# Kernel tuning notes

Hardware: AMD Instinct MI355X
Metric: run time of the kernel (lower is better)

The kernel has to match this reference:

```python
import jax, jax.numpy as jnp
import numpy as np

N = 50000      # nodes
E = 800000     # edges (avg degree 16)
D_IN, D_H, D_OUT = 128, 128, 64
EPS = 1e-5


def setup_inputs() -> dict:
    key = jax.random.key(0)
    ks = jax.random.split(key, 6)
    feat = jax.random.normal(ks[0], (N, D_IN), dtype=jnp.float32)
    # Consistent CSR adjacency: sorted destination rows -> nodePointer via searchsorted
    rows = np.sort(np.asarray(jax.random.randint(ks[1], (E,), 0, N, dtype=jnp.int32)))
    edge_rows = jnp.asarray(rows, dtype=jnp.int32)              # [E] destination node per edge
    nodePointer = jnp.asarray(np.searchsorted(rows, np.arange(N + 1)), dtype=jnp.int32)  # [N+1]
    edgeList = jax.random.randint(ks[2], (E,), 0, N, dtype=jnp.int32)  # [E] source (column) indices
    def glorot(k, i, o):
        return jax.random.normal(k, (i, o), dtype=jnp.float32) * (1.0 / np.sqrt(i)).astype(np.float32)
    W0 = glorot(ks[3], D_IN, D_H)
    W1 = glorot(ks[4], D_H, D_H)
    W2 = glorot(ks[5], D_H, D_OUT)
    return {"feat": feat, "W0": W0, "W1": W1, "W2": W2,
            "nodePointer": nodePointer, "edgeList": edgeList, "edge_rows": edge_rows}


def _layer_norm(x):
    # Fresh nn.LayerNorm each forward in the original => weight=1, bias=0
    mu = jnp.mean(x, axis=-1, keepdims=True)
    var = jnp.mean(jnp.square(x - mu), axis=-1, keepdims=True)
    return (x - mu) * jax.lax.rsqrt(var + EPS)


def reference(feat, W0, W1, W2, nodePointer, edgeList, edge_rows):
    h = feat
    Ws = [W0, W1, W2]
    n_layers = len(Ws)
    for l, W in enumerate(Ws):
        xw = h @ W                      # [N, d_out] dense GEMM
        msg = xw[edgeList]              # [E, d_out] gather source-node features
        h = jax.ops.segment_sum(msg, edge_rows, num_segments=N)  # SpMM: A @ (h W)
        h = _layer_norm(h)
        if l != n_layers - 1:
            h = jax.nn.relu(h)
    return h
```

## Files before the change

### kernel.cpp

```cpp
#include <hip/hip_runtime.h>
#include <cstddef>


typedef __attribute__((ext_vector_type(8))) short bf16x8;
typedef __attribute__((ext_vector_type(4))) float floatx4;
typedef __attribute__((ext_vector_type(4))) unsigned int uintx4;
typedef __attribute__((ext_vector_type(2))) unsigned int uintx2;

static __device__ __forceinline__ unsigned int f2bf(float f) {
    union { float f; unsigned int u; } v; v.f = f;
    unsigned int u = v.u;
    u += 0x7fffu + ((u >> 16) & 1u);
    return u >> 16;
}
static __device__ __forceinline__ float bf_lo(unsigned int p) {
    union { unsigned int u; float f; } v; v.u = p << 16; return v.f;
}
static __device__ __forceinline__ float bf_hi(unsigned int p) {
    union { unsigned int u; float f; } v; v.u = p & 0xffff0000u; return v.f;
}
static __device__ __forceinline__ void acc8(float* a, uintx4 v) {
    a[0] += bf_lo(v.x); a[1] += bf_hi(v.x);
    a[2] += bf_lo(v.y); a[3] += bf_hi(v.y);
    a[4] += bf_lo(v.z); a[5] += bf_hi(v.z);
    a[6] += bf_lo(v.w); a[7] += bf_hi(v.w);
}
static __device__ __forceinline__ void acc4(float* a, uintx2 v) {
    a[0] += bf_lo(v.x); a[1] += bf_hi(v.x);
    a[2] += bf_lo(v.y); a[3] += bf_hi(v.y);
}

__global__ __launch_bounds__(256) void cvt_w(const float* __restrict__ W0,
                                             const float* __restrict__ W1,
                                             const float* __restrict__ W2,
                                             unsigned int* __restrict__ WtF) {
    const int m = blockIdx.x >> 4;
    const int slice = blockIdx.x & 15;
    const float* W = (m == 0) ? W0 : (m == 1) ? W1 : W2;
    const int ncols = (m == 2) ? 64 : 128;
    unsigned int* dst = WtF + m * 128 * 64;
    const int total = ncols * 64;
    for (int idx = slice * 256 + threadIdx.x; idx < total; idx += 16 * 256) {
        const int j    = idx & 3;
        const int lane = (idx >> 2) & 63;
        const int s    = (idx >> 8) & 3;
        const int t    = idx >> 10;
        const int mcol = lane & 15;
        const int quad = lane >> 4;
        const int n = t * 16 + mcol;
        const int k = s * 32 + quad * 8 + 2 * j;
        unsigned int lo = f2bf(W[(size_t)k * ncols + n]);
        unsigned int hi = f2bf(W[(size_t)(k + 1) * ncols + n]);
        dst[idx] = (hi << 16) | lo;
    }
}

template <int NCOLS, bool A_FP32>
__global__ __launch_bounds__(64) void gemm_mfma(const void* __restrict__ Av,
                                                const unsigned int* __restrict__ Wt,
                                                unsigned int* __restrict__ C,
                                                int M) {
    const int lane = threadIdx.x;
    const int row0 = blockIdx.x * 16;
    const int quad = lane >> 4;
    const int mcol = lane & 15;

    constexpr int NT = NCOLS / 16;
    floatx4 acc[NT];
    #pragma unroll
    for (int t = 0; t < NT; ++t) acc[t] = (floatx4){0.f, 0.f, 0.f, 0.f};

    int aidx = row0 + mcol; if (aidx >= M) aidx = M - 1;
    const float*        arowF = (const float*)Av + (size_t)aidx * 128 + quad * 8;
    const unsigned int* afrag = (const unsigned int*)Av + (size_t)blockIdx.x * 1024 + lane * 4;
    const unsigned int* bbase = Wt + lane * 4;

    #pragma unroll
    for (int s = 0; s < 4; ++s) {
        bf16x8 a;
        if constexpr (A_FP32) {
            float4 fa = *(const float4*)(arowF + s * 32);
            float4 fb = *(const float4*)(arowF + s * 32 + 4);
            uintx4 ap;
            ap.x = (f2bf(fa.y) << 16) | f2bf(fa.x);
            ap.y = (f2bf(fa.w) << 16) | f2bf(fa.z);
            ap.z = (f2bf(fb.y) << 16) | f2bf(fb.x);
            ap.w = (f2bf(fb.w) << 16) | f2bf(fb.z);
            a = __builtin_bit_cast(bf16x8, ap);
        } else {
            uintx4 ap = *(const uintx4*)(afrag + s * 256);
            a = __builtin_bit_cast(bf16x8, ap);
        }
        #pragma unroll
        for (int t = 0; t < NT; ++t) {
            uintx4 bp = *(const uintx4*)(bbase + t * 1024 + s * 256);
            bf16x8 b = __builtin_bit_cast(bf16x8, bp);
            acc[t] = __builtin_amdgcn_mfma_f32_16x16x32_bf16(a, b, acc[t], 0, 0, 0);
        }
    }

    const int rowStride = NCOLS >> 1;
    #pragma unroll
    for (int t = 0; t < NT; ++t) {
        #pragma unroll
        for (int r = 0; r < 4; ++r) {
            unsigned int mybf = f2bf(acc[t][r]);
            unsigned int pair = __shfl_xor(mybf, 1, 64);
            int orow = row0 + quad * 4 + r;
            if (orow < M && (mcol & 1) == 0) {
                unsigned int packed = (pair << 16) | mybf;
                C[(size_t)orow * rowStride + t * 8 + (mcol >> 1)] = packed;
            }
        }
    }
}

__global__ __launch_bounds__(256) void agg_ln128(const unsigned int* __restrict__ xw,
                                                 const int* __restrict__ ptr,
                                                 const int* __restrict__ col,
                                                 unsigned int* __restrict__ out,
                                                 int N) {
    const int node = blockIdx.x * 4 + (threadIdx.x >> 6);
    if (node >= N) return;
    const int lane = threadIdx.x & 63;
    const int g  = lane >> 4;
    const int sl = lane & 15;
    const int s = ptr[node];
    const int e = ptr[node + 1];

    float accA[8] = {}, accB[8] = {};
    const unsigned int* base = xw + sl * 4;
    int i = s + g;
    for (; i + 12 < e; i += 16) {
        uintx4 v0 = *(const uintx4*)(base + (size_t)col[i]      * 64);
        uintx4 v1 = *(const uintx4*)(base + (size_t)col[i + 4]  * 64);
        uintx4 v2 = *(const uintx4*)(base + (size_t)col[i + 8]  * 64);
        uintx4 v3 = *(const uintx4*)(base + (size_t)col[i + 12] * 64);
        acc8(accA, v0); acc8(accB, v1); acc8(accA, v2); acc8(accB, v3);
    }
    for (; i < e; i += 4) {
        uintx4 v0 = *(const uintx4*)(base + (size_t)col[i] * 64);
        acc8(accA, v0);
    }

    float acc[8];
    #pragma unroll
    for (int j = 0; j < 8; ++j) acc[j] = accA[j] + accB[j];

    #pragma unroll
    for (int j = 0; j < 8; ++j) {
        acc[j] += __shfl_xor(acc[j], 16, 64);
        acc[j] += __shfl_xor(acc[j], 32, 64);
    }
    float s1 = 0.f, s2 = 0.f;
    #pragma unroll
    for (int j = 0; j < 8; ++j) { s1 += acc[j]; s2 += acc[j] * acc[j]; }
    #pragma unroll
    for (int m = 8; m >= 1; m >>= 1) {
        s1 += __shfl_xor(s1, m, 64);
        s2 += __shfl_xor(s2, m, 64);
    }
    const float mean = s1 * (1.0f / 128.0f);
    const float var  = s2 * (1.0f / 128.0f) - mean * mean;
    const float inv  = rsqrtf(var + 1e-5f);

    if (g == 0) {
        float o[8];
        #pragma unroll
        for (int j = 0; j < 8; ++j)
            o[j] = fmaxf((acc[j] - mean) * inv, 0.f);
        uintx4 p;
        p.x = (f2bf(o[1]) << 16) | f2bf(o[0]);
        p.y = (f2bf(o[3]) << 16) | f2bf(o[2]);
        p.z = (f2bf(o[5]) << 16) | f2bf(o[4]);
        p.w = (f2bf(o[7]) << 16) | f2bf(o[6]);
        const int tile = node >> 4, m = node & 15;
        *(uintx4*)(out + (size_t)tile * 1024 + (sl >> 2) * 256 + (sl & 3) * 64 + m * 4) = p;
    }
}

__global__ __launch_bounds__(256) void agg_ln64(const unsigned int* __restrict__ xw,
                                                const int* __restrict__ ptr,
                                                const int* __restrict__ col,
                                                float* __restrict__ out, int N) {
    const int node = blockIdx.x * 4 + (threadIdx.x >> 6);
    if (node >= N) return;
    const int lane = threadIdx.x & 63;
    const int g  = lane >> 4;
    const int sl = lane & 15;
    const int s = ptr[node];
    const int e = ptr[node + 1];

    float accA[4] = {}, accB[4] = {};
    const unsigned int* base = xw + sl * 2;
    int i = s + g;
    for (; i + 12 < e; i += 16) {
        uintx2 v0 = *(const uintx2*)(base + (size_t)col[i]      * 32);
        uintx2 v1 = *(const uintx2*)(base + (size_t)col[i + 4]  * 32);
        uintx2 v2 = *(const uintx2*)(base + (size_t)col[i + 8]  * 32);
        uintx2 v3 = *(const uintx2*)(base + (size_t)col[i + 12] * 32);
        acc4(accA, v0); acc4(accB, v1); acc4(accA, v2); acc4(accB, v3);
    }
    for (; i < e; i += 4) {
        uintx2 v0 = *(const uintx2*)(base + (size_t)col[i] * 32);
        acc4(accA, v0);
    }

    float acc[4];
    #pragma unroll
    for (int j = 0; j < 4; ++j) acc[j] = accA[j] + accB[j];

    #pragma unroll
    for (int j = 0; j < 4; ++j) {
        acc[j] += __shfl_xor(acc[j], 16, 64);
        acc[j] += __shfl_xor(acc[j], 32, 64);
    }
    float s1 = 0.f, s2 = 0.f;
    #pragma unroll
    for (int j = 0; j < 4; ++j) { s1 += acc[j]; s2 += acc[j] * acc[j]; }
    #pragma unroll
    for (int m = 8; m >= 1; m >>= 1) {
        s1 += __shfl_xor(s1, m, 64);
        s2 += __shfl_xor(s2, m, 64);
    }
    const float mean = s1 * (1.0f / 64.0f);
    const float var  = s2 * (1.0f / 64.0f) - mean * mean;
    const float inv  = rsqrtf(var + 1e-5f);

    if (g == 0) {
        float4 o;
        o.x = (acc[0] - mean) * inv;
        o.y = (acc[1] - mean) * inv;
        o.z = (acc[2] - mean) * inv;
        o.w = (acc[3] - mean) * inv;
        *(float4*)(out + (size_t)node * 64 + sl * 4) = o;
    }
}

extern "C" void kernel_launch(void* const* d_in, const int* in_sizes, int n_in,
                              void* d_out, int out_size, void* d_ws, size_t ws_size,
                              hipStream_t stream) {
    const float* feat = (const float*)d_in[0];
    const float* W0   = (const float*)d_in[1];
    const float* W1   = (const float*)d_in[2];
    const float* W2   = (const float*)d_in[3];
    const int*   ptr  = (const int*)d_in[4];
    const int*   col  = (const int*)d_in[5];

    const int N = in_sizes[4] - 1;

    unsigned int* xwp = (unsigned int*)d_ws;
    unsigned int* hb  = xwp + (size_t)N * 64;
    unsigned int* WtP = hb + (size_t)N * 64;
    float*        out = (float*)d_out;

    const int gemmBlocks = (N + 15) / 16;
    const int nodeBlocks = (N + 3) / 4;

    cvt_w<<<48, 256, 0, stream>>>(W0, W1, W2, WtP);

    gemm_mfma<128, true><<<gemmBlocks, 64, 0, stream>>>(feat, WtP, xwp, N);
    agg_ln128<<<nodeBlocks, 256, 0, stream>>>(xwp, ptr, col, hb, N);
    gemm_mfma<128, false><<<gemmBlocks, 64, 0, stream>>>(hb, WtP + 128 * 64, xwp, N);
    agg_ln128<<<nodeBlocks, 256, 0, stream>>>(xwp, ptr, col, hb, N);
    gemm_mfma<64, false><<<gemmBlocks, 64, 0, stream>>>(hb, WtP + 2 * 128 * 64, xwp, N);
    agg_ln64<<<nodeBlocks, 256, 0, stream>>>(xwp, ptr, col, out, N);
}
```

Baseline: 202.4 us.

## Fuse aggregation+LayerNorm with next layer's MFMA GEMM via LDS tile

Replaces the separate agg_ln128 and gemm_mfma launches with one kernel per 16-node tile. Four waves each aggregate four nodes, apply LayerNorm and ReLU, write bf16 into an LDS tile in MFMA layout, then multiply by the next weight matrix. This removes the global round-trip of the hidden activations and two kernel launches. In exchange each wave handles four nodes serially, which may reduce memory-level parallelism in the gather and adds a block barrier.

```diff
diff --git a/kernel.cpp b/kernel.cpp
--- a/kernel.cpp
+++ b/kernel.cpp
@@ -115,67 +115,114 @@
     }
 }
 
-__global__ __launch_bounds__(256) void agg_ln128(const unsigned int* __restrict__ xw,
-                                                 const int* __restrict__ ptr,
-                                                 const int* __restrict__ col,
-                                                 unsigned int* __restrict__ out,
-                                                 int N) {
-    const int node = blockIdx.x * 4 + (threadIdx.x >> 6);
-    if (node >= N) return;
+template <int NCOLS_OUT>
+__global__ __launch_bounds__(256) void agg_gemm(const unsigned int* __restrict__ xw,
+                                                const int* __restrict__ ptr,
+                                                const int* __restrict__ col,
+                                                const unsigned int* __restrict__ Wt,
+                                                unsigned int* __restrict__ C,
+                                                int N) {
+    __shared__ unsigned int lds[1024];
+    const int tile = blockIdx.x;
+    const int wave = threadIdx.x >> 6;
     const int lane = threadIdx.x & 63;
     const int g  = lane >> 4;
     const int sl = lane & 15;
-    const int s = ptr[node];
-    const int e = ptr[node + 1];
-
-    float accA[8] = {}, accB[8] = {};
+
     const unsigned int* base = xw + sl * 4;
-    int i = s + g;
-    for (; i + 12 < e; i += 16) {
-        uintx4 v0 = *(const uintx4*)(base + (size_t)col[i]      * 64);
-        uintx4 v1 = *(const uintx4*)(base + (size_t)col[i + 4]  * 64);
-        uintx4 v2 = *(const uintx4*)(base + (size_t)col[i + 8]  * 64);
-        uintx4 v3 = *(const uintx4*)(base + (size_t)col[i + 12] * 64);
-        acc8(accA, v0); acc8(accB, v1); acc8(accA, v2); acc8(accB, v3);
-    }
-    for (; i < e; i += 4) {
-        uintx4 v0 = *(const uintx4*)(base + (size_t)col[i] * 64);
-        acc8(accA, v0);
-    }
-
-    float acc[8];
-    #pragma unroll
-    for (int j = 0; j < 8; ++j) acc[j] = accA[j] + accB[j];
-
-    #pragma unroll
-    for (int j = 0; j < 8; ++j) {
-        acc[j] += __shfl_xor(acc[j], 16, 64);
-        acc[j] += __shfl_xor(acc[j], 32, 64);
-    }
-    float s1 = 0.f, s2 = 0.f;
-    #pragma unroll
-    for (int j = 0; j < 8; ++j) { s1 += acc[j]; s2 += acc[j] * acc[j]; }
-    #pragma unroll
-    for (int m = 8; m >= 1; m >>= 1) {
-        s1 += __shfl_xor(s1, m, 64);
-        s2 += __shfl_xor(s2, m, 64);
-    }
-    const float mean = s1 * (1.0f / 128.0f);
-    const float var  = s2 * (1.0f / 128.0f) - mean * mean;
-    const float inv  = rsqrtf(var + 1e-5f);
-
-    if (g == 0) {
-        float o[8];
-        #pragma unroll
-        for (int j = 0; j < 8; ++j)
-            o[j] = fmaxf((acc[j] - mean) * inv, 0.f);
-        uintx4 p;
-        p.x = (f2bf(o[1]) << 16) | f2bf(o[0]);
-        p.y = (f2bf(o[3]) << 16) | f2bf(o[2]);
-        p.z = (f2bf(o[5]) << 16) | f2bf(o[4]);
-        p.w = (f2bf(o[7]) << 16) | f2bf(o[6]);
-        const int tile = node >> 4, m = node & 15;
-        *(uintx4*)(out + (size_t)tile * 1024 + (sl >> 2) * 256 + (sl & 3) * 64 + m * 4) = p;
+    #pragma unroll
+    for (int n = 0; n < 4; ++n) {
+        const int m = wave * 4 + n;
+        const int node = tile * 16 + m;
+        const int nodeC = node < N ? node : N - 1;
+        const int s = ptr[nodeC];
+        const int e = node < N ? ptr[nodeC + 1] : s;
+
+        float accA[8] = {}, accB[8] = {};
+        int i = s + g;
+        for (; i + 12 < e; i += 16) {
+            uintx4 v0 = *(const uintx4*)(base + (size_t)col[i]      * 64);
+            uintx4 v1 = *(const uintx4*)(base + (size_t)col[i + 4]  * 64);
+            uintx4 v2 = *(const uintx4*)(base + (size_t)col[i + 8]  * 64);
+            uintx4 v3 = *(const uintx4*)(base + (size_t)col[i + 12] * 64);
+            acc8(accA, v0); acc8(accB, v1); acc8(accA, v2); acc8(accB, v3);
+        }
+        for (; i < e; i += 4) {
+            uintx4 v0 = *(const uintx4*)(base + (size_t)col[i] * 64);
+            acc8(accA, v0);
+        }
+
+        float acc[8];
+        #pragma unroll
+        for (int j = 0; j < 8; ++j) acc[j] = accA[j] + accB[j];
+
+        #pragma unroll
+        for (int j = 0; j < 8; ++j) {
+            acc[j] += __shfl_xor(acc[j], 16, 64);
+            acc[j] += __shfl_xor(acc[j], 32, 64);
+        }
+        float s1 = 0.f, s2 = 0.f;
+        #pragma unroll
+        for (int j = 0; j < 8; ++j) { s1 += acc[j]; s2 += acc[j] * acc[j]; }
+        #pragma unroll
+        for (int mm = 8; mm >= 1; mm >>= 1) {
+            s1 += __shfl_xor(s1, mm, 64);
+            s2 += __shfl_xor(s2, mm, 64);
+        }
+        const float mean = s1 * (1.0f / 128.0f);
+        const float var  = s2 * (1.0f / 128.0f) - mean * mean;
+        const float inv  = rsqrtf(var + 1e-5f);
+
+        if (g == 0) {
+            float o[8];
+            #pragma unroll
+            for (int j = 0; j < 8; ++j)
+                o[j] = fmaxf((acc[j] - mean) * inv, 0.f);
+            uintx4 p;
+            p.x = (f2bf(o[1]) << 16) | f2bf(o[0]);
+            p.y = (f2bf(o[3]) << 16) | f2bf(o[2]);
+            p.z = (f2bf(o[5]) << 16) | f2bf(o[4]);
+            p.w = (f2bf(o[7]) << 16) | f2bf(o[6]);
+            *(uintx4*)(lds + (sl >> 2) * 256 + (sl & 3) * 64 + m * 4) = p;
+        }
+    }
+    __syncthreads();
+
+    constexpr int WT = NCOLS_OUT / 64;
+    const int quad = lane >> 4;
+    const int mcol = lane & 15;
+    floatx4 acc[WT];
+    #pragma unroll
+    for (int t = 0; t < WT; ++t) acc[t] = (floatx4){0.f, 0.f, 0.f, 0.f};
+
+    const unsigned int* bbase = Wt + lane * 4;
+    #pragma unroll
+    for (int s4 = 0; s4 < 4; ++s4) {
+        uintx4 ap = *(const uintx4*)(lds + s4 * 256 + lane * 4);
+        bf16x8 a = __builtin_bit_cast(bf16x8, ap);
+        #pragma unroll
+        for (int tt = 0; tt < WT; ++tt) {
+            const int t = wave * WT + tt;
+            uintx4 bp = *(const uintx4*)(bbase + t * 1024 + s4 * 256);
+            bf16x8 b = __builtin_bit_cast(bf16x8, bp);
+            acc[tt] = __builtin_amdgcn_mfma_f32_16x16x32_bf16(a, b, acc[tt], 0, 0, 0);
+        }
+    }
+
+    const int rowStride = NCOLS_OUT >> 1;
+    #pragma unroll
+    for (int tt = 0; tt < WT; ++tt) {
+        const int t = wave * WT + tt;
+        #pragma unroll
+        for (int r = 0; r < 4; ++r) {
+            unsigned int mybf = f2bf(acc[tt][r]);
+            unsigned int pair = __shfl_xor(mybf, 1, 64);
+            const int orow = tile * 16 + quad * 4 + r;
+            if (orow < N && (mcol & 1) == 0) {
+                unsigned int packed = (pair << 16) | mybf;
+                C[(size_t)orow * rowStride + t * 8 + (mcol >> 1)] = packed;
+            }
+        }
     }
 }
 
@@ -249,20 +296,18 @@
 
     const int N = in_sizes[4] - 1;
 
-    unsigned int* xwp = (unsigned int*)d_ws;
-    unsigned int* hb  = xwp + (size_t)N * 64;
-    unsigned int* WtP = hb + (size_t)N * 64;
-    float*        out = (float*)d_out;
+    unsigned int* buf0 = (unsigned int*)d_ws;
+    unsigned int* buf1 = buf0 + (size_t)N * 64;
+    unsigned int* WtP  = buf1 + (size_t)N * 64;
+    float*        out  = (float*)d_out;
 
     const int gemmBlocks = (N + 15) / 16;
     const int nodeBlocks = (N + 3) / 4;
 
     cvt_w<<<48, 256, 0, stream>>>(W0, W1, W2, WtP);
 
-    gemm_mfma<128, true><<<gemmBlocks, 64, 0, stream>>>(feat, WtP, xwp, N);
-    agg_ln128<<<nodeBlocks, 256, 0, stream>>>(xwp, ptr, col, hb, N);
-    gemm_mfma<128, false><<<gemmBlocks, 64, 0, stream>>>(hb, WtP + 128 * 64, xwp, N);
-    agg_ln128<<<nodeBlocks, 256, 0, stream>>>(xwp, ptr, col, hb, N);
-    gemm_mfma<64, false><<<gemmBlocks, 64, 0, stream>>>(hb, WtP + 2 * 128 * 64, xwp, N);
-    agg_ln64<<<nodeBlocks, 256, 0, stream>>>(xwp, ptr, col, out, N);
-}
+    gemm_mfma<128, true><<<gemmBlocks, 64, 0, stream>>>(feat, WtP, buf0, N);
+    agg_gemm<128><<<gemmBlocks, 256, 0, stream>>>(buf0, ptr, col, WtP + 128 * 64, buf1, N);
+    agg_gemm<64><<<gemmBlocks, 256, 0, stream>>>(buf1, ptr, col, WtP + 2 * 128 * 64, buf0, N);
+    agg_ln64<<<nodeBlocks, 256, 0, stream>>>(buf0, ptr, col, out, N);
+}
```

Result: no change. 198.6 us (-1.9%).
